# Kernel optimization log

Hardware: AMD Instinct MI355X
Metric: run time of the kernel (lower is better)

The kernel has to match this reference:

```python
import jax, jax.numpy as jnp
import numpy as np

B, OBS, TASK = 65536, 512, 128
D, M, N = 64, 32, 4  # embedding dim, module width, modules per layer


def setup_inputs() -> dict:
    key = jax.random.key(0)
    ks = jax.random.split(key, 16)

    def w(k, shape):
        fan_in = shape[-2]
        return jax.random.normal(k, shape, jnp.float32) * np.float32(np.sqrt(2.0 / fan_in))

    z = lambda *s: jnp.zeros(s, jnp.float32)
    return dict(
        obs=jax.random.normal(ks[0], (B, OBS), jnp.float32),
        task=jax.random.normal(ks[1], (B, TASK), jnp.float32),
        Ws1=w(ks[2], (OBS, D)), bs1=z(D),
        Ws2=w(ks[3], (D, D)), bs2=z(D),
        Wt=w(ks[4], (TASK, D)), bt=z(D),
        Wa0=w(ks[5], (D, N * N)), ba0=z(N * N),
        Wa1=w(ks[6], (D, N * N)), ba1=z(N * N),
        Wc0=w(ks[7], (N * N, D)), bc0=z(D),
        Wc1=w(ks[8], (2 * N * N, D)), bc1=z(D),
        We0=w(ks[9], (N, D, M)), be0=z(N, M),
        We1=w(ks[10], (N, M, M)), be1=z(N, M),
        We2=w(ks[11], (N, M, M)), be2=z(N, M),
    )


def reference(obs, task, Ws1, bs1, Ws2, bs2, Wt, bt, Wa0, ba0, Wa1, ba1,
              Wc0, bc0, Wc1, bc1, We0, be0, We1, be1, We2, be2):
    relu = jax.nn.relu
    # base encoders
    s = relu(relu(obs @ Ws1 + bs1) @ Ws2 + bs2)          # [B, D]
    t = relu(task @ Wt + bt)                              # [B, D]
    r0 = s * t                                            # first routing inputs [B, D]
    prev = jnp.broadcast_to(s[None], (N,) + s.shape)      # [N, B, D] (state emb fed to all layer-0 modules)

    # routing layer 0 -> 1
    a0 = jax.nn.softmax((r0 @ Wa0 + ba0).reshape(-1, N, N), axis=-1)   # [B, N_next, N_prev]
    m = relu(jnp.einsum('nbi,nio->nbo', prev, We0) + be0[:, None, :])  # [N, B, M] expert outputs
    prev = jnp.einsum('bij,jbd->ibd', a0, m)                           # [N, B, M] attention-combined
    r = relu((a0.reshape(-1, N * N) @ Wc0 + bc0) * r0)                 # updated routing inputs

    # routing layer 1 -> 2
    a1 = jax.nn.softmax((r @ Wa1 + ba1).reshape(-1, N, N), axis=-1)
    m = relu(jnp.einsum('nbi,nio->nbo', prev, We1) + be1[:, None, :])
    prev = jnp.einsum('bij,jbd->ibd', a1, m)
    attn_cat = jnp.concatenate([a0.reshape(-1, N * N), a1.reshape(-1, N * N)], axis=-1)
    r = relu((attn_cat @ Wc1 + bc1) * r0)  # computed as in original (unused afterward)

    # final module layer, plain sum over modules
    m = relu(jnp.einsum('nbi,nio->nbo', prev, We2) + be2[:, None, :])  # [N, B, M]
    return relu(m.sum(axis=0))                                          # [B, M]
```

## Files before the change

### kernel.cpp

```cpp
#include <hip/hip_runtime.h>
#include <hip/hip_bf16.h>


using f32x4 = __attribute__((ext_vector_type(4))) float;
using h16x4 = __attribute__((ext_vector_type(4))) _Float16;
using h16x8 = __attribute__((ext_vector_type(8))) _Float16;
using u32x4 = __attribute__((ext_vector_type(4))) unsigned int;
using u32x2 = __attribute__((ext_vector_type(2))) unsigned int;

#define MFMA16(a, b, c) __builtin_amdgcn_mfma_f32_16x16x16f16((a), (b), (c), 0, 0, 0)

__device__ __forceinline__ short h_bits(float f) {
  _Float16 h = (_Float16)f;
  return __builtin_bit_cast(short, h);
}

__device__ __forceinline__ void dma16(const void* g, char* l) {
  __builtin_amdgcn_global_load_lds(
      (const __attribute__((address_space(1))) unsigned int*)g,
      (__attribute__((address_space(3))) unsigned int*)l, 16, 0, 0);
}

__global__ void sm_convert_v16(
    const float* __restrict__ Ws1, const float* __restrict__ Ws2, const float* __restrict__ Wt,
    const float* __restrict__ Wa0, const float* __restrict__ Wa1, const float* __restrict__ Wc0,
    const float* __restrict__ We0, const float* __restrict__ We1, const float* __restrict__ We2,
    const float* __restrict__ bs1, const float* __restrict__ bs2, const float* __restrict__ bt,
    const float* __restrict__ ba0, const float* __restrict__ ba1, const float* __restrict__ bc0,
    const float* __restrict__ be0, const float* __restrict__ be1, const float* __restrict__ be2,
    short* __restrict__ wsh, float* __restrict__ biasf) {
  int d = blockIdx.x * 256 + threadIdx.x;
  if (d < 64512) {
    float v;
    if (d < 32768) {
      int kk   = d & 3;
      int ntip = (d >> 2) & 1;
      int p    = (d >> 3) & 15;
      int q    = (d >> 7) & 3;
      int pair = (d >> 9) & 1;
      int kb2  = (d >> 10) & 1;
      int c    = d >> 11;
      int k = c * 32 + kb2 * 16 + q * 4 + kk;
      int o = pair * 32 + ntip * 16 + p;
      v = Ws1[k * 64 + o];
    }
    else if (d < 36864) { int r = d - 32768, o = r >> 6, k = r & 63;   v = Ws2[k * 64 + o]; }
    else if (d < 45056) {
      int r = d - 36864;
      int kk   = r & 3;
      int ntip = (r >> 2) & 1;
      int p    = (r >> 3) & 15;
      int q    = (r >> 7) & 3;
      int pair = (r >> 9) & 1;
      int kb2  = (r >> 10) & 1;
      int c    = r >> 11;
      int k = c * 32 + kb2 * 16 + q * 4 + kk;
      int o = pair * 32 + ntip * 16 + p;
      v = Wt[k * 64 + o];
    }
    else if (d < 46080) { int r = d - 45056, o = r >> 6, k = r & 63;   v = Wa0[k * 16 + o]; }
    else if (d < 47104) { int r = d - 46080, o = r >> 6, k = r & 63;   v = Wa1[k * 16 + o]; }
    else if (d < 48128) { int r = d - 47104, o = r >> 4, k = r & 15;   v = Wc0[k * 64 + o]; }
    else if (d < 56320) { int r = d - 48128, n = r >> 11, o = (r >> 6) & 31, i = r & 63; v = We0[n * 2048 + i * 32 + o]; }
    else if (d < 60416) { int r = d - 56320, n = r >> 10, o = (r >> 5) & 31, i = r & 31; v = We1[n * 1024 + i * 32 + o]; }
    else                { int r = d - 60416, n = r >> 10, o = (r >> 5) & 31, i = r & 31; v = We2[n * 1024 + i * 32 + o]; }
    wsh[d] = h_bits(v);
  } else if (d < 65184) {
    int r = d - 64512;
    float v;
    if      (r < 64)  v = bs1[r];
    else if (r < 128) v = bs2[r - 64];
    else if (r < 192) v = bt[r - 128];
    else if (r < 208) v = ba0[r - 192];
    else if (r < 224) v = ba1[r - 208];
    else if (r < 288) v = bc0[r - 224];
    else if (r < 416) v = be0[r - 288];
    else if (r < 544) v = be1[r - 416];
    else              v = be2[r - 544];
    biasf[r] = v;
  }
}

__global__ __launch_bounds__(64) void sm_fused_v16(
    const float* __restrict__ obs, const float* __restrict__ task,
    const short* __restrict__ wsh, const float* __restrict__ biasf,
    float* __restrict__ out) {
  const int lane = threadIdx.x & 63;
  const int q    = lane >> 4;
  const int p    = lane & 15;
  const int rowblk = blockIdx.x * 16;

  __shared__ __align__(16) char lds[15232];
  char* x_lds  = lds;
  char* a_lds  = lds + 2176;
  char* ring   = lds + 2944;
  char* pm_lds = lds + 2944;

  const short* Bp1  = wsh;
  const short* Ws2T = wsh + 32768;
  const short* WtP  = wsh + 36864;
  const short* Wa0T = wsh + 45056;
  const short* Wa1T = wsh + 46080;
  const short* Wc0T = wsh + 47104;
  const short* We0T = wsh + 48128;
  const short* We1T = wsh + 56320;
  const short* We2T = wsh + 60416;
  const float* bs1 = biasf;        const float* bs2 = biasf + 64;
  const float* bt  = biasf + 128;  const float* ba0 = biasf + 192;
  const float* ba1 = biasf + 208;  const float* bc0 = biasf + 224;
  const float* be0 = biasf + 288;  const float* be1 = biasf + 416;
  const float* be2 = biasf + 544;

  const f32x4 z4 = {0.f, 0.f, 0.f, 0.f};

  auto stx  = [&](int row, int col, float v) { *(short*)(x_lds + row * 136 + col * 2) = h_bits(v); };
  auto ldx4 = [&](int row, int k0) -> h16x4 { return *(const h16x4*)(x_lds + row * 136 + k0 * 2); };
  auto ldb  = [&](const short* W, int off) -> h16x4 { return *(const h16x4*)(W + off); };
  auto cvtA = [&](const u32x4& u) -> h16x4 {
    float4 v = __builtin_bit_cast(float4, u);
    h16x4 a;
    a[0] = (_Float16)v.x; a[1] = (_Float16)v.y;
    a[2] = (_Float16)v.z; a[3] = (_Float16)v.w;
    return a;
  };
  auto lo2 = [&](const u32x4& u) -> h16x4 { return __builtin_bit_cast(h16x4, (u32x2){u[0], u[1]}); };
  auto hi2 = [&](const u32x4& u) -> h16x4 { return __builtin_bit_cast(h16x4, (u32x2){u[2], u[3]}); };

  auto stageA = [&](const float* base, int rowlen, int k0, int buf) {
#pragma unroll
    for (int j = 0; j < 2; ++j) {
      int f = j * 64 + lane;
      int row = f >> 3;
      int cl = (f & 7) ^ (row & 7);
      dma16(base + (size_t)(rowblk + row) * rowlen + k0 + cl * 4,
            ring + buf * 6144 + j * 1024);
    }
  };
  auto stageB = [&](const short* bsrc, int c, int buf) {
#pragma unroll
    for (int j = 0; j < 4; ++j)
      dma16((const char*)bsrc + c * 4096 + (j * 64 + lane) * 16,
            ring + buf * 6144 + 2048 + j * 1024);
  };
  auto lda_ = [&](int buf, int kb2) -> u32x4 {
    return *(const u32x4*)(ring + buf * 6144 + p * 128 +
                           (((kb2 * 4 + q) ^ (p & 7)) * 16));
  };
  auto ldbs = [&](int buf, int kb2, int pair) -> u32x4 {
    return *(const u32x4*)(ring + buf * 6144 + 2048 + kb2 * 2048 + pair * 1024 + lane * 16);
  };

  f32x4 accX[4] = {z4, z4, z4, z4};
  {
    stageA(obs, 512, 0, 0); stageB(Bp1, 0, 0);
    for (int c = 0; c < 16; ++c) {
      if (c + 1 < 16) {
        stageA(obs, 512, (c + 1) * 32, (c + 1) & 1);
        stageB(Bp1, c + 1, (c + 1) & 1);
        __builtin_amdgcn_sched_barrier(0);
        asm volatile("s_waitcnt vmcnt(6)" ::: "memory");
      } else {
        asm volatile("s_waitcnt vmcnt(0)" ::: "memory");
      }
      __builtin_amdgcn_sched_barrier(0);
      const int buf = c & 1;
#pragma unroll
      for (int kb2 = 0; kb2 < 2; ++kb2) {
        h16x4 a = cvtA(lda_(buf, kb2));
        u32x4 B0 = ldbs(buf, kb2, 0);
        u32x4 B1 = ldbs(buf, kb2, 1);
        accX[0] = MFMA16(a, lo2(B0), accX[0]);
        accX[1] = MFMA16(a, hi2(B0), accX[1]);
        accX[2] = MFMA16(a, lo2(B1), accX[2]);
        accX[3] = MFMA16(a, hi2(B1), accX[3]);
      }
    }
  }

  stageA(task, 128, 0, 0); stageB(WtP, 0, 0);

#pragma unroll
  for (int nt = 0; nt < 4; ++nt) {
    float bias = bs1[nt * 16 + p];
#pragma unroll
    for (int r = 0; r < 4; ++r)
      stx(4 * q + r, nt * 16 + p, fmaxf(accX[nt][r] + bias, 0.f));
  }

  f32x4 accS[4] = {z4, z4, z4, z4};
#pragma unroll
  for (int kb = 0; kb < 4; ++kb) {
    h16x4 a = ldx4(p, kb * 16 + q * 4);
#pragma unroll
    for (int nt = 0; nt < 4; ++nt)
      accS[nt] = MFMA16(a, ldb(Ws2T, (nt * 16 + p) * 64 + kb * 16 + q * 4), accS[nt]);
  }
  float sf[4][4];
#pragma unroll
  for (int nt = 0; nt < 4; ++nt) {
    float bias = bs2[nt * 16 + p];
#pragma unroll
    for (int r = 0; r < 4; ++r) sf[nt][r] = fmaxf(accS[nt][r] + bias, 0.f);
  }
#pragma unroll
  for (int nt = 0; nt < 4; ++nt)
#pragma unroll
    for (int r = 0; r < 4; ++r) stx(4 * q + r, nt * 16 + p, sf[nt][r]);

  f32x4 accT[4] = {z4, z4, z4, z4};
  {
    for (int c = 0; c < 4; ++c) {
      if (c + 1 < 4) {
        stageA(task, 128, (c + 1) * 32, (c + 1) & 1);
        stageB(WtP, c + 1, (c + 1) & 1);
        __builtin_amdgcn_sched_barrier(0);
        asm volatile("s_waitcnt vmcnt(6)" ::: "memory");
      } else {
        asm volatile("s_waitcnt vmcnt(0)" ::: "memory");
      }
      __builtin_amdgcn_sched_barrier(0);
      const int buf = c & 1;
#pragma unroll
      for (int kb2 = 0; kb2 < 2; ++kb2) {
        h16x4 a = cvtA(lda_(buf, kb2));
        u32x4 B0 = ldbs(buf, kb2, 0);
        u32x4 B1 = ldbs(buf, kb2, 1);
        accT[0] = MFMA16(a, lo2(B0), accT[0]);
        accT[1] = MFMA16(a, hi2(B0), accT[1]);
        accT[2] = MFMA16(a, lo2(B1), accT[2]);
        accT[3] = MFMA16(a, hi2(B1), accT[3]);
      }
    }
  }
  float r0f[4][4];
#pragma unroll
  for (int nt = 0; nt < 4; ++nt) {
    float bias = bt[nt * 16 + p];
#pragma unroll
    for (int r = 0; r < 4; ++r)
      r0f[nt][r] = sf[nt][r] * fmaxf(accT[nt][r] + bias, 0.f);
  }

  float mfr[4][2][4];
#pragma unroll
  for (int n = 0; n < 4; ++n) {
    f32x4 acc[2] = {z4, z4};
#pragma unroll
    for (int kb = 0; kb < 4; ++kb) {
      h16x4 a = ldx4(p, kb * 16 + q * 4);
#pragma unroll
      for (int nt = 0; nt < 2; ++nt)
        acc[nt] = MFMA16(a, ldb(We0T, (n * 32 + nt * 16 + p) * 64 + kb * 16 + q * 4), acc[nt]);
    }
#pragma unroll
    for (int nt = 0; nt < 2; ++nt) {
      float bias = be0[n * 32 + nt * 16 + p];
#pragma unroll
      for (int r = 0; r < 4; ++r) mfr[n][nt][r] = fmaxf(acc[nt][r] + bias, 0.f);
    }
  }

#pragma unroll
  for (int nt = 0; nt < 4; ++nt)
#pragma unroll
    for (int r = 0; r < 4; ++r) stx(4 * q + r, nt * 16 + p, r0f[nt][r]);

  f32x4 accA = z4;
#pragma unroll
  for (int kb = 0; kb < 4; ++kb)
    accA = MFMA16(ldx4(p, kb * 16 + q * 4), ldb(Wa0T, p * 64 + kb * 16 + q * 4), accA);
  float a0v[4];
  {
    float bias = ba0[p];
#pragma unroll
    for (int r = 0; r < 4; ++r) {
      float v = accA[r] + bias;
      float mx = fmaxf(v, __shfl_xor(v, 1));
      mx = fmaxf(mx, __shfl_xor(mx, 2));
      float e = __expf(v - mx);
      float ssum = e + __shfl_xor(e, 1);
      ssum += __shfl_xor(ssum, 2);
      a0v[r] = e / ssum;
    }
  }
#pragma unroll
  for (int r = 0; r < 4; ++r)
    *(short*)(a_lds + (4 * q + r) * 48 + p * 2) = h_bits(a0v[r]);

  float pv[4][2][4];
#pragma unroll
  for (int r = 0; r < 4; ++r) {
    h16x8 alo = *(const h16x8*)(a_lds + (4 * q + r) * 48);
    h16x8 ahi = *(const h16x8*)(a_lds + (4 * q + r) * 48 + 16);
    float av[16];
#pragma unroll
    for (int e = 0; e < 8; ++e) { av[e] = (float)alo[e]; av[8 + e] = (float)ahi[e]; }
#pragma unroll
    for (int i = 0; i < 4; ++i) {
      float s0 = 0.f, s1 = 0.f;
#pragma unroll
      for (int j = 0; j < 4; ++j) {
        s0 += av[4 * i + j] * mfr[j][0][r];
        s1 += av[4 * i + j] * mfr[j][1][r];
      }
      pv[i][0][r] = s0; pv[i][1][r] = s1;
    }
  }

  f32x4 accC[4] = {z4, z4, z4, z4};
  {
    h16x4 a = *(const h16x4*)(a_lds + p * 48 + q * 8);
#pragma unroll
    for (int nt = 0; nt < 4; ++nt)
      accC[nt] = MFMA16(a, ldb(Wc0T, (nt * 16 + p) * 16 + q * 4), accC[nt]);
  }
  float rf[4][4];
#pragma unroll
  for (int nt = 0; nt < 4; ++nt) {
    float bias = bc0[nt * 16 + p];
#pragma unroll
    for (int r = 0; r < 4; ++r)
      rf[nt][r] = fmaxf((accC[nt][r] + bias) * r0f[nt][r], 0.f);
  }
#pragma unroll
  for (int nt = 0; nt < 4; ++nt)
#pragma unroll
    for (int r = 0; r < 4; ++r) stx(4 * q + r, nt * 16 + p, rf[nt][r]);

  f32x4 accA1 = z4;
#pragma unroll
  for (int kb = 0; kb < 4; ++kb)
    accA1 = MFMA16(ldx4(p, kb * 16 + q * 4), ldb(Wa1T, p * 64 + kb * 16 + q * 4), accA1);
  float a1v[4];
  {
    float bias = ba1[p];
#pragma unroll
    for (int r = 0; r < 4; ++r) {
      float v = accA1[r] + bias;
      float mx = fmaxf(v, __shfl_xor(v, 1));
      mx = fmaxf(mx, __shfl_xor(mx, 2));
      float e = __expf(v - mx);
      float ssum = e + __shfl_xor(e, 1);
      ssum += __shfl_xor(ssum, 2);
      a1v[r] = e / ssum;
    }
  }

#pragma unroll
  for (int i = 0; i < 4; ++i)
#pragma unroll
    for (int nt = 0; nt < 2; ++nt)
#pragma unroll
      for (int r = 0; r < 4; ++r)
        *(short*)(pm_lds + (i * 16 + 4 * q + r) * 80 + (nt * 16 + p) * 2) = h_bits(pv[i][nt][r]);

  float m1f[4][2][4];
#pragma unroll
  for (int n = 0; n < 4; ++n) {
    f32x4 acc[2] = {z4, z4};
#pragma unroll
    for (int kb = 0; kb < 2; ++kb) {
      h16x4 a = *(const h16x4*)(pm_lds + (n * 16 + p) * 80 + kb * 32 + q * 8);
#pragma unroll
      for (int nt = 0; nt < 2; ++nt)
        acc[nt] = MFMA16(a, ldb(We1T, (n * 32 + nt * 16 + p) * 32 + kb * 16 + q * 4), acc[nt]);
    }
#pragma unroll
    for (int nt = 0; nt < 2; ++nt) {
      float bias = be1[n * 32 + nt * 16 + p];
#pragma unroll
      for (int r = 0; r < 4; ++r) m1f[n][nt][r] = fmaxf(acc[nt][r] + bias, 0.f);
    }
  }

  float pv2[4][2][4];
#pragma unroll
  for (int r = 0; r < 4; ++r) {
    float av[16];
#pragma unroll
    for (int cc = 0; cc < 16; ++cc)
      av[cc] = __shfl(a1v[r], (lane & 48) | cc);
#pragma unroll
    for (int i = 0; i < 4; ++i) {
      float s0 = 0.f, s1 = 0.f;
#pragma unroll
      for (int j = 0; j < 4; ++j) {
        s0 += av[4 * i + j] * m1f[j][0][r];
        s1 += av[4 * i + j] * m1f[j][1][r];
      }
      pv2[i][0][r] = s0; pv2[i][1][r] = s1;
    }
  }

#pragma unroll
  for (int i = 0; i < 4; ++i)
#pragma unroll
    for (int nt = 0; nt < 2; ++nt)
#pragma unroll
      for (int r = 0; r < 4; ++r)
        *(short*)(pm_lds + (i * 16 + 4 * q + r) * 80 + (nt * 16 + p) * 2) = h_bits(pv2[i][nt][r]);

  float of[2][4] = {{0.f, 0.f, 0.f, 0.f}, {0.f, 0.f, 0.f, 0.f}};
#pragma unroll
  for (int n = 0; n < 4; ++n) {
    f32x4 acc[2] = {z4, z4};
#pragma unroll
    for (int kb = 0; kb < 2; ++kb) {
      h16x4 a = *(const h16x4*)(pm_lds + (n * 16 + p) * 80 + kb * 32 + q * 8);
#pragma unroll
      for (int nt = 0; nt < 2; ++nt)
        acc[nt] = MFMA16(a, ldb(We2T, (n * 32 + nt * 16 + p) * 32 + kb * 16 + q * 4), acc[nt]);
    }
#pragma unroll
    for (int nt = 0; nt < 2; ++nt) {
      float bias = be2[n * 32 + nt * 16 + p];
#pragma unroll
      for (int r = 0; r < 4; ++r) of[nt][r] += fmaxf(acc[nt][r] + bias, 0.f);
    }
  }
#pragma unroll
  for (int nt = 0; nt < 2; ++nt)
#pragma unroll
    for (int r = 0; r < 4; ++r) {
      int grow = rowblk + 4 * q + r;
      out[(size_t)grow * 32 + nt * 16 + p] = of[nt][r];
    }
}

extern "C" void kernel_launch(void* const* d_in, const int* in_sizes, int n_in,
                              void* d_out, int out_size, void* d_ws, size_t ws_size,
                              hipStream_t stream) {
  (void)in_sizes; (void)n_in; (void)out_size; (void)ws_size;
  const float* obs  = (const float*)d_in[0];
  const float* task = (const float*)d_in[1];
  const float* Ws1 = (const float*)d_in[2];  const float* bs1 = (const float*)d_in[3];
  const float* Ws2 = (const float*)d_in[4];  const float* bs2 = (const float*)d_in[5];
  const float* Wt  = (const float*)d_in[6];  const float* bt  = (const float*)d_in[7];
  const float* Wa0 = (const float*)d_in[8];  const float* ba0 = (const float*)d_in[9];
  const float* Wa1 = (const float*)d_in[10]; const float* ba1 = (const float*)d_in[11];
  const float* Wc0 = (const float*)d_in[12]; const float* bc0 = (const float*)d_in[13];
  const float* We0 = (const float*)d_in[16]; const float* be0 = (const float*)d_in[17];
  const float* We1 = (const float*)d_in[18]; const float* be1 = (const float*)d_in[19];
  const float* We2 = (const float*)d_in[20]; const float* be2 = (const float*)d_in[21];

  short* wsh   = (short*)d_ws;
  float* biasf = (float*)((char*)d_ws + 129040);

  sm_convert_v16<<<dim3(255), dim3(256), 0, stream>>>(
      Ws1, Ws2, Wt, Wa0, Wa1, Wc0, We0, We1, We2,
      bs1, bs2, bt, ba0, ba1, bc0, be0, be1, be2,
      wsh, biasf);
  sm_fused_v16<<<dim3(4096), dim3(64), 0, stream>>>(
      obs, task, wsh, biasf, (float*)d_out);
}
```

Measured before the change: 79.02 us.

## Process two 16-row tiles per wave to reuse staged weight chunks

Each single-wave block now handles 32 batch rows instead of 16. The obs/Ws1 and task/Wt streaming GEMMs reuse each staged B chunk for two A tiles, which halves weight DMA traffic per row and doubles MFMA work per barrier. The routing tail then loops over the two tiles. The cost is more accumulator registers, a larger LDS ring, and half as many blocks, which could lower occupancy and latency hiding.

```diff
diff --git a/kernel.cpp b/kernel.cpp
--- a/kernel.cpp
+++ b/kernel.cpp
@@ -21,7 +21,7 @@
       (__attribute__((address_space(3))) unsigned int*)l, 16, 0, 0);
 }
 
-__global__ void sm_convert_v16(
+__global__ void sm_convert_v17(
     const float* __restrict__ Ws1, const float* __restrict__ Ws2, const float* __restrict__ Wt,
     const float* __restrict__ Wa0, const float* __restrict__ Wa1, const float* __restrict__ Wc0,
     const float* __restrict__ We0, const float* __restrict__ We1, const float* __restrict__ We2,
@@ -81,16 +81,16 @@
   }
 }
 
-__global__ __launch_bounds__(64) void sm_fused_v16(
+__global__ __launch_bounds__(64) void sm_fused_v17(
     const float* __restrict__ obs, const float* __restrict__ task,
     const short* __restrict__ wsh, const float* __restrict__ biasf,
     float* __restrict__ out) {
   const int lane = threadIdx.x & 63;
   const int q    = lane >> 4;
   const int p    = lane & 15;
-  const int rowblk = blockIdx.x * 16;
-
-  __shared__ __align__(16) char lds[15232];
+  const int rowblk = blockIdx.x * 32;
+
+  __shared__ __align__(16) char lds[19328];
   char* x_lds  = lds;
   char* a_lds  = lds + 2176;
   char* ring   = lds + 2944;
@@ -128,29 +128,29 @@
 
   auto stageA = [&](const float* base, int rowlen, int k0, int buf) {
 #pragma unroll
-    for (int j = 0; j < 2; ++j) {
+    for (int j = 0; j < 4; ++j) {
       int f = j * 64 + lane;
       int row = f >> 3;
       int cl = (f & 7) ^ (row & 7);
       dma16(base + (size_t)(rowblk + row) * rowlen + k0 + cl * 4,
-            ring + buf * 6144 + j * 1024);
+            ring + buf * 8192 + j * 1024);
     }
   };
   auto stageB = [&](const short* bsrc, int c, int buf) {
 #pragma unroll
     for (int j = 0; j < 4; ++j)
       dma16((const char*)bsrc + c * 4096 + (j * 64 + lane) * 16,
-            ring + buf * 6144 + 2048 + j * 1024);
+            ring + buf * 8192 + 4096 + j * 1024);
   };
-  auto lda_ = [&](int buf, int kb2) -> u32x4 {
-    return *(const u32x4*)(ring + buf * 6144 + p * 128 +
+  auto lda_ = [&](int buf, int kb2, int t) -> u32x4 {
+    return *(const u32x4*)(ring + buf * 8192 + (p + 16 * t) * 128 +
                            (((kb2 * 4 + q) ^ (p & 7)) * 16));
   };
   auto ldbs = [&](int buf, int kb2, int pair) -> u32x4 {
-    return *(const u32x4*)(ring + buf * 6144 + 2048 + kb2 * 2048 + pair * 1024 + lane * 16);
+    return *(const u32x4*)(ring + buf * 8192 + 4096 + kb2 * 2048 + pair * 1024 + lane * 16);
   };
 
-  f32x4 accX[4] = {z4, z4, z4, z4};
+  f32x4 accX[2][4] = {{z4, z4, z4, z4}, {z4, z4, z4, z4}};
   {
     stageA(obs, 512, 0, 0); stageB(Bp1, 0, 0);
     for (int c = 0; c < 16; ++c) {
@@ -158,7 +158,7 @@
         stageA(obs, 512, (c + 1) * 32, (c + 1) & 1);
         stageB(Bp1, c + 1, (c + 1) & 1);
         __builtin_amdgcn_sched_barrier(0);
-        asm volatile("s_waitcnt vmcnt(6)" ::: "memory");
+        asm volatile("s_waitcnt vmcnt(8)" ::: "memory");
       } else {
         asm volatile("s_waitcnt vmcnt(0)" ::: "memory");
       }
@@ -166,55 +166,30 @@
       const int buf = c & 1;
 #pragma unroll
       for (int kb2 = 0; kb2 < 2; ++kb2) {
-        h16x4 a = cvtA(lda_(buf, kb2));
         u32x4 B0 = ldbs(buf, kb2, 0);
         u32x4 B1 = ldbs(buf, kb2, 1);
-        accX[0] = MFMA16(a, lo2(B0), accX[0]);
-        accX[1] = MFMA16(a, hi2(B0), accX[1]);
-        accX[2] = MFMA16(a, lo2(B1), accX[2]);
-        accX[3] = MFMA16(a, hi2(B1), accX[3]);
+#pragma unroll
+        for (int t = 0; t < 2; ++t) {
+          h16x4 a = cvtA(lda_(buf, kb2, t));
+          accX[t][0] = MFMA16(a, lo2(B0), accX[t][0]);
+          accX[t][1] = MFMA16(a, hi2(B0), accX[t][1]);
+          accX[t][2] = MFMA16(a, lo2(B1), accX[t][2]);
+          accX[t][3] = MFMA16(a, hi2(B1), accX[t][3]);
+        }
       }
     }
   }
 
   stageA(task, 128, 0, 0); stageB(WtP, 0, 0);
 
-#pragma unroll
-  for (int nt = 0; nt < 4; ++nt) {
-    float bias = bs1[nt * 16 + p];
-#pragma unroll
-    for (int r = 0; r < 4; ++r)
-      stx(4 * q + r, nt * 16 + p, fmaxf(accX[nt][r] + bias, 0.f));
-  }
-
-  f32x4 accS[4] = {z4, z4, z4, z4};
-#pragma unroll
-  for (int kb = 0; kb < 4; ++kb) {
-    h16x4 a = ldx4(p, kb * 16 + q * 4);
-#pragma unroll
-    for (int nt = 0; nt < 4; ++nt)
-      accS[nt] = MFMA16(a, ldb(Ws2T, (nt * 16 + p) * 64 + kb * 16 + q * 4), accS[nt]);
-  }
-  float sf[4][4];
-#pragma unroll
-  for (int nt = 0; nt < 4; ++nt) {
-    float bias = bs2[nt * 16 + p];
-#pragma unroll
-    for (int r = 0; r < 4; ++r) sf[nt][r] = fmaxf(accS[nt][r] + bias, 0.f);
-  }
-#pragma unroll
-  for (int nt = 0; nt < 4; ++nt)
-#pragma unroll
-    for (int r = 0; r < 4; ++r) stx(4 * q + r, nt * 16 + p, sf[nt][r]);
-
-  f32x4 accT[4] = {z4, z4, z4, z4};
+  f32x4 accT[2][4] = {{z4, z4, z4, z4}, {z4, z4, z4, z4}};
   {
     for (int c = 0; c < 4; ++c) {
       if (c + 1 < 4) {
         stageA(task, 128, (c + 1) * 32, (c + 1) & 1);
         stageB(WtP, c + 1, (c + 1) & 1);
         __builtin_amdgcn_sched_barrier(0);
-        asm volatile("s_waitcnt vmcnt(6)" ::: "memory");
+        asm volatile("s_waitcnt vmcnt(8)" ::: "memory");
       } else {
         asm volatile("s_waitcnt vmcnt(0)" ::: "memory");
       }
@@ -222,209 +197,246 @@
       const int buf = c & 1;
 #pragma unroll
       for (int kb2 = 0; kb2 < 2; ++kb2) {
-        h16x4 a = cvtA(lda_(buf, kb2));
         u32x4 B0 = ldbs(buf, kb2, 0);
         u32x4 B1 = ldbs(buf, kb2, 1);
-        accT[0] = MFMA16(a, lo2(B0), accT[0]);
-        accT[1] = MFMA16(a, hi2(B0), accT[1]);
-        accT[2] = MFMA16(a, lo2(B1), accT[2]);
-        accT[3] = MFMA16(a, hi2(B1), accT[3]);
+#pragma unroll
+        for (int t = 0; t < 2; ++t) {
+          h16x4 a = cvtA(lda_(buf, kb2, t));
+          accT[t][0] = MFMA16(a, lo2(B0), accT[t][0]);
+          accT[t][1] = MFMA16(a, hi2(B0), accT[t][1]);
+          accT[t][2] = MFMA16(a, lo2(B1), accT[t][2]);
+          accT[t][3] = MFMA16(a, hi2(B1), accT[t][3]);
+        }
       }
     }
   }
-  float r0f[4][4];
-#pragma unroll
-  for (int nt = 0; nt < 4; ++nt) {
-    float bias = bt[nt * 16 + p];
-#pragma unroll
-    for (int r = 0; r < 4; ++r)
-      r0f[nt][r] = sf[nt][r] * fmaxf(accT[nt][r] + bias, 0.f);
-  }
-
-  float mfr[4][2][4];
-#pragma unroll
-  for (int n = 0; n < 4; ++n) {
-    f32x4 acc[2] = {z4, z4};
+
+#pragma unroll
+  for (int t = 0; t < 2; ++t) {
+    const int trow = rowblk + 16 * t;
+
+#pragma unroll
+    for (int nt = 0; nt < 4; ++nt) {
+      float bias = bs1[nt * 16 + p];
+#pragma unroll
+      for (int r = 0; r < 4; ++r)
+        stx(4 * q + r, nt * 16 + p, fmaxf(accX[t][nt][r] + bias, 0.f));
+    }
+
+    f32x4 accS[4] = {z4, z4, z4, z4};
 #pragma unroll
     for (int kb = 0; kb < 4; ++kb) {
       h16x4 a = ldx4(p, kb * 16 + q * 4);
 #pragma unroll
+      for (int nt = 0; nt < 4; ++nt)
+        accS[nt] = MFMA16(a, ldb(Ws2T, (nt * 16 + p) * 64 + kb * 16 + q * 4), accS[nt]);
+    }
+    float sf[4][4];
+#pragma unroll
+    for (int nt = 0; nt < 4; ++nt) {
+      float bias = bs2[nt * 16 + p];
+#pragma unroll
+      for (int r = 0; r < 4; ++r) sf[nt][r] = fmaxf(accS[nt][r] + bias, 0.f);
+    }
+#pragma unroll
+    for (int nt = 0; nt < 4; ++nt)
+#pragma unroll
+      for (int r = 0; r < 4; ++r) stx(4 * q + r, nt * 16 + p, sf[nt][r]);
+
+    float r0f[4][4];
+#pragma unroll
+    for (int nt = 0; nt < 4; ++nt) {
+      float bias = bt[nt * 16 + p];
+#pragma unroll
+      for (int r = 0; r < 4; ++r)
+        r0f[nt][r] = sf[nt][r] * fmaxf(accT[t][nt][r] + bias, 0.f);
+    }
+
+    float mfr[4][2][4];
+#pragma unroll
+    for (int n = 0; n < 4; ++n) {
+      f32x4 acc[2] = {z4, z4};
+#pragma unroll
+      for (int kb = 0; kb < 4; ++kb) {
+        h16x4 a = ldx4(p, kb * 16 + q * 4);
+#pragma unroll
+        for (int nt = 0; nt < 2; ++nt)
+          acc[nt] = MFMA16(a, ldb(We0T, (n * 32 + nt * 16 + p) * 64 + kb * 16 + q * 4), acc[nt]);
+      }
+#pragma unroll
+      for (int nt = 0; nt < 2; ++nt) {
+        float bias = be0[n * 32 + nt * 16 + p];
+#pragma unroll
+        for (int r = 0; r < 4; ++r) mfr[n][nt][r] = fmaxf(acc[nt][r] + bias, 0.f);
+      }
+    }
+
+#pragma unroll
+    for (int nt = 0; nt < 4; ++nt)
+#pragma unroll
+      for (int r = 0; r < 4; ++r) stx(4 * q + r, nt * 16 + p, r0f[nt][r]);
+
+    f32x4 accA = z4;
+#pragma unroll
+    for (int kb = 0; kb < 4; ++kb)
+      accA = MFMA16(ldx4(p, kb * 16 + q * 4), ldb(Wa0T, p * 64 + kb * 16 + q * 4), accA);
+    float a0v[4];
+    {
+      float bias = ba0[p];
+#pragma unroll
+      for (int r = 0; r < 4; ++r) {
+        float v = accA[r] + bias;
+        float mx = fmaxf(v, __shfl_xor(v, 1));
+        mx = fmaxf(mx, __shfl_xor(mx, 2));
+        float e = __expf(v - mx);
+        float ssum = e + __shfl_xor(e, 1);
+        ssum += __shfl_xor(ssum, 2);
+        a0v[r] = e / ssum;
+      }
+    }
+#pragma unroll
+    for (int r = 0; r < 4; ++r)
+      *(short*)(a_lds + (4 * q + r) * 48 + p * 2) = h_bits(a0v[r]);
+
+    float pv[4][2][4];
+#pragma unroll
+    for (int r = 0; r < 4; ++r) {
+      h16x8 alo = *(const h16x8*)(a_lds + (4 * q + r) * 48);
+      h16x8 ahi = *(const h16x8*)(a_lds + (4 * q + r) * 48 + 16);
+      float av[16];
+#pragma unroll
+      for (int e = 0; e < 8; ++e) { av[e] = (float)alo[e]; av[8 + e] = (float)ahi[e]; }
+#pragma unroll
+      for (int i = 0; i < 4; ++i) {
+        float s0 = 0.f, s1 = 0.f;
+#pragma unroll
+        for (int j = 0; j < 4; ++j) {
+          s0 += av[4 * i + j] * mfr[j][0][r];
+          s1 += av[4 * i + j] * mfr[j][1][r];
+        }
+        pv[i][0][r] = s0; pv[i][1][r] = s1;
+      }
+    }
+
+    f32x4 accC[4] = {z4, z4, z4, z4};
+    {
+      h16x4 a = *(const h16x4*)(a_lds + p * 48 + q * 8);
+#pragma unroll
+      for (int nt = 0; nt < 4; ++nt)
+        accC[nt] = MFMA16(a, ldb(Wc0T, (nt * 16 + p) * 16 + q * 4), accC[nt]);
+    }
+    float rf[4][4];
+#pragma unroll
+    for (int nt = 0; nt < 4; ++nt) {
+      float bias = bc0[nt * 16 + p];
+#pragma unroll
+      for (int r = 0; r < 4; ++r)
+        rf[nt][r] = fmaxf((accC[nt][r] + bias) * r0f[nt][r], 0.f);
+    }
+#pragma unroll
+    for (int nt = 0; nt < 4; ++nt)
+#pragma unroll
+      for (int r = 0; r < 4; ++r) stx(4 * q + r, nt * 16 + p, rf[nt][r]);
+
+    f32x4 accA1 = z4;
+#pragma unroll
+    for (int kb = 0; kb < 4; ++kb)
+      accA1 = MFMA16(ldx4(p, kb * 16 + q * 4), ldb(Wa1T, p * 64 + kb * 16 + q * 4), accA1);
+    float a1v[4];
+    {
+      float bias = ba1[p];
+#pragma unroll
+      for (int r = 0; r < 4; ++r) {
+        float v = accA1[r] + bias;
+        float mx = fmaxf(v, __shfl_xor(v, 1));
+        mx = fmaxf(mx, __shfl_xor(mx, 2));
+        float e = __expf(v - mx);
+        float ssum = e + __shfl_xor(e, 1);
+        ssum += __shfl_xor(ssum, 2);
+        a1v[r] = e / ssum;
+      }
+    }
+
+#pragma unroll
+    for (int i = 0; i < 4; ++i)
+#pragma unroll
       for (int nt = 0; nt < 2; ++nt)
-        acc[nt] = MFMA16(a, ldb(We0T, (n * 32 + nt * 16 + p) * 64 + kb * 16 + q * 4), acc[nt]);
-    }
-#pragma unroll
-    for (int nt = 0; nt < 2; ++nt) {
-      float bias = be0[n * 32 + nt * 16 + p];
-#pragma unroll
-      for (int r = 0; r < 4; ++r) mfr[n][nt][r] = fmaxf(acc[nt][r] + bias, 0.f);
-    }
+#pragma unroll
+        for (int r = 0; r < 4; ++r)
+          *(short*)(pm_lds + (i * 16 + 4 * q + r) * 80 + (nt * 16 + p) * 2) = h_bits(pv[i][nt][r]);
+
+    float m1f[4][2][4];
+#pragma unroll
+    for (int n = 0; n < 4; ++n) {
+      f32x4 acc[2] = {z4, z4};
+#pragma unroll
+      for (int kb = 0; kb < 2; ++kb) {
+        h16x4 a = *(const h16x4*)(pm_lds + (n * 16 + p) * 80 + kb * 32 + q * 8);
+#pragma unroll
+        for (int nt = 0; nt < 2; ++nt)
+          acc[nt] = MFMA16(a, ldb(We1T, (n * 32 + nt * 16 + p) * 32 + kb * 16 + q * 4), acc[nt]);
+      }
+#pragma unroll
+      for (int nt = 0; nt < 2; ++nt) {
+        float bias = be1[n * 32 + nt * 16 + p];
+#pragma unroll
+        for (int r = 0; r < 4; ++r) m1f[n][nt][r] = fmaxf(acc[nt][r] + bias, 0.f);
+      }
+    }
+
+    float pv2[4][2][4];
+#pragma unroll
+    for (int r = 0; r < 4; ++r) {
+      float av[16];
+#pragma unroll
+      for (int cc = 0; cc < 16; ++cc)
+        av[cc] = __shfl(a1v[r], (lane & 48) | cc);
+#pragma unroll
+      for (int i = 0; i < 4; ++i) {
+        float s0 = 0.f, s1 = 0.f;
+#pragma unroll
+        for (int j = 0; j < 4; ++j) {
+          s0 += av[4 * i + j] * m1f[j][0][r];
+          s1 += av[4 * i + j] * m1f[j][1][r];
+        }
+        pv2[i][0][r] = s0; pv2[i][1][r] = s1;
+      }
+    }
+
+#pragma unroll
+    for (int i = 0; i < 4; ++i)
+#pragma unroll
+      for (int nt = 0; nt < 2; ++nt)
+#pragma unroll
+        for (int r = 0; r < 4; ++r)
+          *(short*)(pm_lds + (i * 16 + 4 * q + r) * 80 + (nt * 16 + p) * 2) = h_bits(pv2[i][nt][r]);
+
+    float of[2][4] = {{0.f, 0.f, 0.f, 0.f}, {0.f, 0.f, 0.f, 0.f}};
+#pragma unroll
+    for (int n = 0; n < 4; ++n) {
+      f32x4 acc[2] = {z4, z4};
+#pragma unroll
+      for (int kb = 0; kb < 2; ++kb) {
+        h16x4 a = *(const h16x4*)(pm_lds + (n * 16 + p) * 80 + kb * 32 + q * 8);
+#pragma unroll
+        for (int nt = 0; nt < 2; ++nt)
+          acc[nt] = MFMA16(a, ldb(We2T, (n * 32 + nt * 16 + p) * 32 + kb * 16 + q * 4), acc[nt]);
+      }
+#pragma unroll
+      for (int nt = 0; nt < 2; ++nt) {
+        float bias = be2[n * 32 + nt * 16 + p];
+#pragma unroll
+        for (int r = 0; r < 4; ++r) of[nt][r] += fmaxf(acc[nt][r] + bias, 0.f);
+      }
+    }
+#pragma unroll
+    for (int nt = 0; nt < 2; ++nt)
+#pragma unroll
+      for (int r = 0; r < 4; ++r) {
+        int grow = trow + 4 * q + r;
+        out[(size_t)grow * 32 + nt * 16 + p] = of[nt][r];
+      }
   }
-
-#pragma unroll
-  for (int nt = 0; nt < 4; ++nt)
-#pragma unroll
-    for (int r = 0; r < 4; ++r) stx(4 * q + r, nt * 16 + p, r0f[nt][r]);
-
-  f32x4 accA = z4;
-#pragma unroll
-  for (int kb = 0; kb < 4; ++kb)
-    accA = MFMA16(ldx4(p, kb * 16 + q * 4), ldb(Wa0T, p * 64 + kb * 16 + q * 4), accA);
-  float a0v[4];
-  {
-    float bias = ba0[p];
-#pragma unroll
-    for (int r = 0; r < 4; ++r) {
-      float v = accA[r] + bias;
-      float mx = fmaxf(v, __shfl_xor(v, 1));
-      mx = fmaxf(mx, __shfl_xor(mx, 2));
-      float e = __expf(v - mx);
-      float ssum = e + __shfl_xor(e, 1);
-      ssum += __shfl_xor(ssum, 2);
-      a0v[r] = e / ssum;
-    }
-  }
-#pragma unroll
-  for (int r = 0; r < 4; ++r)
-    *(short*)(a_lds + (4 * q + r) * 48 + p * 2) = h_bits(a0v[r]);
-
-  float pv[4][2][4];
-#pragma unroll
-  for (int r = 0; r < 4; ++r) {
-    h16x8 alo = *(const h16x8*)(a_lds + (4 * q + r) * 48);
-    h16x8 ahi = *(const h16x8*)(a_lds + (4 * q + r) * 48 + 16);
-    float av[16];
-#pragma unroll
-    for (int e = 0; e < 8; ++e) { av[e] = (float)alo[e]; av[8 + e] = (float)ahi[e]; }
-#pragma unroll
-    for (int i = 0; i < 4; ++i) {
-      float s0 = 0.f, s1 = 0.f;
-#pragma unroll
-      for (int j = 0; j < 4; ++j) {
-        s0 += av[4 * i + j] * mfr[j][0][r];
-        s1 += av[4 * i + j] * mfr[j][1][r];
-      }
-      pv[i][0][r] = s0; pv[i][1][r] = s1;
-    }
-  }
-
-  f32x4 accC[4] = {z4, z4, z4, z4};
-  {
-    h16x4 a = *(const h16x4*)(a_lds + p * 48 + q * 8);
-#pragma unroll
-    for (int nt = 0; nt < 4; ++nt)
-      accC[nt] = MFMA16(a, ldb(Wc0T, (nt * 16 + p) * 16 + q * 4), accC[nt]);
-  }
-  float rf[4][4];
-#pragma unroll
-  for (int nt = 0; nt < 4; ++nt) {
-    float bias = bc0[nt * 16 + p];
-#pragma unroll
-    for (int r = 0; r < 4; ++r)
-      rf[nt][r] = fmaxf((accC[nt][r] + bias) * r0f[nt][r], 0.f);
-  }
-#pragma unroll
-  for (int nt = 0; nt < 4; ++nt)
-#pragma unroll
-    for (int r = 0; r < 4; ++r) stx(4 * q + r, nt * 16 + p, rf[nt][r]);
-
-  f32x4 accA1 = z4;
-#pragma unroll
-  for (int kb = 0; kb < 4; ++kb)
-    accA1 = MFMA16(ldx4(p, kb * 16 + q * 4), ldb(Wa1T, p * 64 + kb * 16 + q * 4), accA1);
-  float a1v[4];
-  {
-    float bias = ba1[p];
-#pragma unroll
-    for (int r = 0; r < 4; ++r) {
-      float v = accA1[r] + bias;
-      float mx = fmaxf(v, __shfl_xor(v, 1));
-      mx = fmaxf(mx, __shfl_xor(mx, 2));
-      float e = __expf(v - mx);
-      float ssum = e + __shfl_xor(e, 1);
-      ssum += __shfl_xor(ssum, 2);
-      a1v[r] = e / ssum;
-    }
-  }
-
-#pragma unroll
-  for (int i = 0; i < 4; ++i)
-#pragma unroll
-    for (int nt = 0; nt < 2; ++nt)
-#pragma unroll
-      for (int r = 0; r < 4; ++r)
-        *(short*)(pm_lds + (i * 16 + 4 * q + r) * 80 + (nt * 16 + p) * 2) = h_bits(pv[i][nt][r]);
-
-  float m1f[4][2][4];
-#pragma unroll
-  for (int n = 0; n < 4; ++n) {
-    f32x4 acc[2] = {z4, z4};
-#pragma unroll
-    for (int kb = 0; kb < 2; ++kb) {
-      h16x4 a = *(const h16x4*)(pm_lds + (n * 16 + p) * 80 + kb * 32 + q * 8);
-#pragma unroll
-      for (int nt = 0; nt < 2; ++nt)
-        acc[nt] = MFMA16(a, ldb(We1T, (n * 32 + nt * 16 + p) * 32 + kb * 16 + q * 4), acc[nt]);
-    }
-#pragma unroll
-    for (int nt = 0; nt < 2; ++nt) {
-      float bias = be1[n * 32 + nt * 16 + p];
-#pragma unroll
-      for (int r = 0; r < 4; ++r) m1f[n][nt][r] = fmaxf(acc[nt][r] + bias, 0.f);
-    }
-  }
-
-  float pv2[4][2][4];
-#pragma unroll
-  for (int r = 0; r < 4; ++r) {
-    float av[16];
-#pragma unroll
-    for (int cc = 0; cc < 16; ++cc)
-      av[cc] = __shfl(a1v[r], (lane & 48) | cc);
-#pragma unroll
-    for (int i = 0; i < 4; ++i) {
-      float s0 = 0.f, s1 = 0.f;
-#pragma unroll
-      for (int j = 0; j < 4; ++j) {
-        s0 += av[4 * i + j] * m1f[j][0][r];
-        s1 += av[4 * i + j] * m1f[j][1][r];
-      }
-      pv2[i][0][r] = s0; pv2[i][1][r] = s1;
-    }
-  }
-
-#pragma unroll
-  for (int i = 0; i < 4; ++i)
-#pragma unroll
-    for (int nt = 0; nt < 2; ++nt)
-#pragma unroll
-      for (int r = 0; r < 4; ++r)
-        *(short*)(pm_lds + (i * 16 + 4 * q + r) * 80 + (nt * 16 + p) * 2) = h_bits(pv2[i][nt][r]);
-
-  float of[2][4] = {{0.f, 0.f, 0.f, 0.f}, {0.f, 0.f, 0.f, 0.f}};
-#pragma unroll
-  for (int n = 0; n < 4; ++n) {
-    f32x4 acc[2] = {z4, z4};
-#pragma unroll
-    for (int kb = 0; kb < 2; ++kb) {
-      h16x4 a = *(const h16x4*)(pm_lds + (n * 16 + p) * 80 + kb * 32 + q * 8);
-#pragma unroll
-      for (int nt = 0; nt < 2; ++nt)
-        acc[nt] = MFMA16(a, ldb(We2T, (n * 32 + nt * 16 + p) * 32 + kb * 16 + q * 4), acc[nt]);
-    }
-#pragma unroll
-    for (int nt = 0; nt < 2; ++nt) {
-      float bias = be2[n * 32 + nt * 16 + p];
-#pragma unroll
-      for (int r = 0; r < 4; ++r) of[nt][r] += fmaxf(acc[nt][r] + bias, 0.f);
-    }
-  }
-#pragma unroll
-  for (int nt = 0; nt < 2; ++nt)
-#pragma unroll
-    for (int r = 0; r < 4; ++r) {
-      int grow = rowblk + 4 * q + r;
-      out[(size_t)grow * 32 + nt * 16 + p] = of[nt][r];
-    }
 }
 
 extern "C" void kernel_launch(void* const* d_in, const int* in_sizes, int n_in,
@@ -446,10 +458,10 @@
   short* wsh   = (short*)d_ws;
   float* biasf = (float*)((char*)d_ws + 129040);
 
-  sm_convert_v16<<<dim3(255), dim3(256), 0, stream>>>(
+  sm_convert_v17<<<dim3(255), dim3(256), 0, stream>>>(
       Ws1, Ws2, Wt, Wa0, Wa1, Wc0, We0, We1, We2,
       bs1, bs2, bt, ba0, ba1, bc0, be0, be1, be2,
       wsh, biasf);
-  sm_fused_v16<<<dim3(4096), dim3(64), 0, stream>>>(
+  sm_fused_v17<<<dim3(2048), dim3(64), 0, stream>>>(
       obs, task, wsh, biasf, (float*)d_out);
 }
```

Result: faster. 75.04 us (-5.0%).
